# Kernel optimization log

Measured on AMD Instinct MI355X. Metric: run time of the kernel, lower is better.

## Reference

```python
import math
import jax, jax.numpy as jnp
import numpy as np

STEP, BSIZE, NNOD, DIM, HID = 32, 4096, 8, 64, 64


def setup_inputs() -> dict:
    key = jax.random.key(0)
    ks = jax.random.split(key, 9)
    s = 1.0 / math.sqrt(HID)  # torch default uniform init scale
    inp = {
        "input": jax.random.normal(ks[0], (STEP, BSIZE, NNOD, DIM), dtype=jnp.float32),
        "time_dis": jax.random.uniform(ks[1], (BSIZE, STEP), dtype=jnp.float32) * 5.0,
        "w_ih": jax.random.uniform(ks[2], (4 * HID, DIM), jnp.float32, -s, s),
        "w_hh": jax.random.uniform(ks[3], (4 * HID, HID), jnp.float32, -s, s),
        "b_ih": jax.random.uniform(ks[4], (4 * HID,), jnp.float32, -s, s),
        "b_hh": jax.random.uniform(ks[5], (4 * HID,), jnp.float32, -s, s),
        "fc2_w": jax.random.uniform(ks[6], (1, HID), jnp.float32, -s, s),
        "fc2_b": jax.random.uniform(ks[7], (1,), jnp.float32, -s, s),
        "baseline": jnp.array([-30.0], dtype=jnp.float32),
    }
    return inp


def reference(input, time_dis, w_ih, w_hh, b_ih, b_hh, fc2_w, fc2_b, baseline):
    step, bsize, num_nodule, dim = input.shape
    bn = bsize * num_nodule
    x = input.reshape(step, bn, dim)                       # [S, B*N, D]
    # time_dis: [B, S] -> expand over nodules -> [S, B*N]
    td = jnp.broadcast_to(time_dis[:, :, None], (bsize, step, num_nodule))
    td = jnp.transpose(td, (1, 0, 2)).reshape(step, bn)
    # original loop: step 0 uses td[0], step i>0 uses td[i-1]
    td_used = jnp.concatenate([td[:1], td[:-1]], axis=0)   # [S, B*N]

    hid = w_hh.shape[1]
    h0 = jnp.zeros((bn, hid), dtype=input.dtype)
    c0 = jnp.zeros((bn, hid), dtype=input.dtype)

    def cell(carry, step_in):
        h, c = carry
        x_t, t_t = step_in
        gates = x_t @ w_ih.T + b_ih + h @ w_hh.T + b_hh    # [B*N, 4H]
        i_g, f_g, g_g, o_g = jnp.split(gates, 4, axis=-1)
        i_g = jax.nn.sigmoid(i_g)
        f_g = jax.nn.sigmoid(f_g)
        g_g = jnp.tanh(g_g)
        o_g = jax.nn.sigmoid(o_g)
        # time-distanced decay on the retained cell memory: 1/log(e + dt)
        decay = (1.0 / jnp.log(math.e + t_t))[:, None]
        c_new = f_g * decay * c + i_g * g_g
        h_new = o_g * jnp.tanh(c_new)
        return (h_new, c_new), None

    (hx, cx), _ = jax.lax.scan(cell, (h0, c0), (x, td_used))

    out2 = jax.nn.sigmoid(hx @ fc2_w.T + fc2_b).reshape(bsize, num_nodule)
    base_prob = jax.nn.sigmoid(baseline)[0]
    # noisy-OR pooling over nodules plus learned baseline leak
    casePred = 1.0 - jnp.prod(1.0 - out2, axis=1) * (1.0 - base_prob)
    return casePred
```

## Files before the change

kernel.cpp:

```cpp
#include <hip/hip_runtime.h>
#include <hip/hip_bf16.h>
#include <math.h>


#define STEPS 32
#define BSIZE 4096
#define NNOD  8
#define DIMK  64
#define HIDK  64
#define BN    (BSIZE * NNOD)
#define ROWS  64
#define NBLK  (BN / ROWS)

typedef __attribute__((ext_vector_type(8))) short short8;
typedef __attribute__((ext_vector_type(4))) float f32x4;

__device__ __forceinline__ unsigned short f2bf(float f) {
    union { float f; unsigned u; } v; v.f = f;
    unsigned r = v.u + 0x7fffu + ((v.u >> 16) & 1u);
    return (unsigned short)(r >> 16);
}
__device__ __forceinline__ float bf2f(unsigned short h) {
    union { unsigned u; float f; } v; v.u = ((unsigned)h) << 16;
    return v.f;
}
__device__ __forceinline__ float fast_sigmoid(float x) {
    float e = __builtin_amdgcn_exp2f(-1.44269504f * x);
    return __builtin_amdgcn_rcpf(1.0f + e);
}
__device__ __forceinline__ float fast_tanh(float x) {
    float e = __builtin_amdgcn_exp2f(2.88539008f * x);
    return 1.0f - 2.0f * __builtin_amdgcn_rcpf(e + 1.0f);
}

__global__ __launch_bounds__(256, 2)
void disrnn_kernel(const float* __restrict__ x,
                   const float* __restrict__ time_dis,
                   const float* __restrict__ w_ih,
                   const float* __restrict__ w_hh,
                   const float* __restrict__ b_ih,
                   const float* __restrict__ b_hh,
                   const float* __restrict__ fc2_w,
                   const float* __restrict__ fc2_b,
                   const float* __restrict__ baseline,
                   float* __restrict__ out)
{
    __shared__ unsigned short sX[ROWS * 64];
    __shared__ unsigned short sH[ROWS * 64];
    __shared__ float sDecay[8 * STEPS];

    const int tid  = threadIdx.x;
    const int wave = tid >> 6;
    const int lane = tid & 63;
    const int l15  = lane & 15;
    const int lk   = lane >> 4;
    const int blk  = blockIdx.x;
    const int row0 = blk * ROWS;

    {
        int g = tid >> 5, st = tid & 31;
        int b = blk * 8 + g;
        float td = time_dis[b * STEPS + (st == 0 ? 0 : st - 1)];
        sDecay[g * STEPS + st] = __builtin_amdgcn_rcpf(logf(2.71828182845904523f + td));
    }
    for (int i = tid; i < ROWS * 64; i += 256) sH[i] = 0;

    short8 bwih[4][2], bwhh[4][2];
    float  biasv[4];
    #pragma unroll
    for (int q = 0; q < 4; ++q) {
        int n = q * 64 + wave * 16 + l15;
        biasv[q] = b_ih[n] + b_hh[n];
        #pragma unroll
        for (int kk = 0; kk < 2; ++kk) {
            int k0 = kk * 32 + lk * 8;
            short8 vi, vh;
            #pragma unroll
            for (int j = 0; j < 8; ++j) {
                vi[j] = (short)f2bf(w_ih[n * 64 + k0 + j]);
                vh[j] = (short)f2bf(w_hh[n * 64 + k0 + j]);
            }
            bwih[q][kk] = vi;
            bwhh[q][kk] = vh;
        }
    }

    float c[4][4];
    #pragma unroll
    for (int m = 0; m < 4; ++m)
        #pragma unroll
        for (int j = 0; j < 4; ++j) c[m][j] = 0.0f;

    __syncthreads();

    for (int s = 0; s < STEPS; ++s) {
        const float* Xs = x + ((size_t)s * BN + row0) * DIMK;
        #pragma unroll
        for (int it = 0; it < 2; ++it) {
            int gg = it * 256 + tid;
            int r  = gg >> 3, ch = gg & 7;
            const float4* src = (const float4*)(Xs + r * 64 + ch * 8);
            float4 a = src[0], b2 = src[1];
            short8 v;
            v[0] = (short)f2bf(a.x);  v[1] = (short)f2bf(a.y);
            v[2] = (short)f2bf(a.z);  v[3] = (short)f2bf(a.w);
            v[4] = (short)f2bf(b2.x); v[5] = (short)f2bf(b2.y);
            v[6] = (short)f2bf(b2.z); v[7] = (short)f2bf(b2.w);
            *(short8*)&sX[r * 64 + ((ch ^ (r & 7)) * 8)] = v;
        }
        __syncthreads();

        f32x4 acc[4][4];
        #pragma unroll
        for (int m = 0; m < 4; ++m) {
            int rl = m * 16 + l15;
            int sw = rl & 7;
            short8 ax0 = *(const short8*)&sX[rl * 64 + (((0 + lk) ^ sw) * 8)];
            short8 ax1 = *(const short8*)&sX[rl * 64 + (((4 + lk) ^ sw) * 8)];
            short8 ah0 = *(const short8*)&sH[rl * 64 + (((0 + lk) ^ sw) * 8)];
            short8 ah1 = *(const short8*)&sH[rl * 64 + (((4 + lk) ^ sw) * 8)];
            #pragma unroll
            for (int q = 0; q < 4; ++q) {
                f32x4 a0 = {biasv[q], biasv[q], biasv[q], biasv[q]};
                a0 = __builtin_amdgcn_mfma_f32_16x16x32_bf16(ax0, bwih[q][0], a0, 0, 0, 0);
                a0 = __builtin_amdgcn_mfma_f32_16x16x32_bf16(ax1, bwih[q][1], a0, 0, 0, 0);
                a0 = __builtin_amdgcn_mfma_f32_16x16x32_bf16(ah0, bwhh[q][0], a0, 0, 0, 0);
                a0 = __builtin_amdgcn_mfma_f32_16x16x32_bf16(ah1, bwhh[q][1], a0, 0, 0, 0);
                acc[m][q] = a0;
            }
        }
        __syncthreads();

        #pragma unroll
        for (int m = 0; m < 4; ++m) {
            #pragma unroll
            for (int j = 0; j < 4; ++j) {
                int rl = m * 16 + lk * 4 + j;
                float decay = sDecay[(rl >> 3) * STEPS + s];
                float ig = fast_sigmoid(acc[m][0][j]);
                float fg = fast_sigmoid(acc[m][1][j]);
                float g2 = fast_tanh(acc[m][2][j]);
                float og = fast_sigmoid(acc[m][3][j]);
                float cn = fg * decay * c[m][j] + ig * g2;
                c[m][j] = cn;
                float hn = og * fast_tanh(cn);
                int col = wave * 16 + l15;
                sH[rl * 64 + (((col >> 3) ^ (rl & 7)) * 8) + (col & 7)] = f2bf(hn);
            }
        }
    }
    __syncthreads();

    if (tid < 64) {
        int r = tid;
        float sum = 0.0f;
        #pragma unroll
        for (int ch = 0; ch < 8; ++ch) {
            short8 v = *(const short8*)&sH[r * 64 + ((ch ^ (r & 7)) * 8)];
            #pragma unroll
            for (int j = 0; j < 8; ++j)
                sum += bf2f((unsigned short)v[j]) * fc2_w[ch * 8 + j];
        }
        float p  = fast_sigmoid(sum + fc2_b[0]);
        float qv = 1.0f - p;
        qv *= __shfl_xor(qv, 1);
        qv *= __shfl_xor(qv, 2);
        qv *= __shfl_xor(qv, 4);
        if ((tid & 7) == 0) {
            float bp = fast_sigmoid(baseline[0]);
            out[blk * 8 + (tid >> 3)] = 1.0f - qv * (1.0f - bp);
        }
    }
}

extern "C" void kernel_launch(void* const* d_in, const int* in_sizes, int n_in,
                              void* d_out, int out_size, void* d_ws, size_t ws_size,
                              hipStream_t stream) {
    const float* x        = (const float*)d_in[0];
    const float* time_dis = (const float*)d_in[1];
    const float* w_ih     = (const float*)d_in[2];
    const float* w_hh     = (const float*)d_in[3];
    const float* b_ih     = (const float*)d_in[4];
    const float* b_hh     = (const float*)d_in[5];
    const float* fc2_w    = (const float*)d_in[6];
    const float* fc2_b    = (const float*)d_in[7];
    const float* baseline = (const float*)d_in[8];
    float* out = (float*)d_out;

    disrnn_kernel<<<dim3(NBLK), dim3(256), 0, stream>>>(
        x, time_dis, w_ih, w_hh, b_ih, b_hh, fc2_w, fc2_b, baseline, out);
}
```

Baseline: 398.6 us.

## Prefetch next timestep input into registers and use LDS-only barriers

Loads the next step's x tile into registers while the current step computes, then converts and stores it to LDS at the top of the following iteration. Replaces __syncthreads with a barrier that waits only on LDS counters, so the in-flight global prefetch is not drained at each sync. Also hoists the decay lookup out of the inner loop. Adds register pressure under the 2-blocks-per-CU launch bound.

```diff
diff --git a/kernel.cpp b/kernel.cpp
--- a/kernel.cpp
+++ b/kernel.cpp
@@ -31,6 +31,11 @@
 __device__ __forceinline__ float fast_tanh(float x) {
     float e = __builtin_amdgcn_exp2f(2.88539008f * x);
     return 1.0f - 2.0f * __builtin_amdgcn_rcpf(e + 1.0f);
+}
+__device__ __forceinline__ void block_sync_lds() {
+    asm volatile("s_waitcnt lgkmcnt(0)" ::: "memory");
+    __builtin_amdgcn_s_barrier();
+    asm volatile("" ::: "memory");
 }
 
 __global__ __launch_bounds__(256, 2)
@@ -57,6 +62,18 @@
     const int blk  = blockIdx.x;
     const int row0 = blk * ROWS;
 
+    const int r0 = tid >> 3,        c0 = tid & 7;
+    const int r1 = (256 + tid) >> 3, c1 = tid & 7;
+
+    float4 pa0, pa1, pb0, pb1;
+    {
+        const float* Xs = x + (size_t)row0 * DIMK;
+        const float* s0 = Xs + r0 * 64 + c0 * 8;
+        const float* s1 = Xs + r1 * 64 + c1 * 8;
+        pa0 = ((const float4*)s0)[0]; pa1 = ((const float4*)s0)[1];
+        pb0 = ((const float4*)s1)[0]; pb1 = ((const float4*)s1)[1];
+    }
+
     {
         int g = tid >> 5, st = tid & 31;
         int b = blk * 8 + g;
@@ -91,24 +108,31 @@
         #pragma unroll
         for (int j = 0; j < 4; ++j) c[m][j] = 0.0f;
 
-    __syncthreads();
+    block_sync_lds();
 
     for (int s = 0; s < STEPS; ++s) {
-        const float* Xs = x + ((size_t)s * BN + row0) * DIMK;
-        #pragma unroll
-        for (int it = 0; it < 2; ++it) {
-            int gg = it * 256 + tid;
-            int r  = gg >> 3, ch = gg & 7;
-            const float4* src = (const float4*)(Xs + r * 64 + ch * 8);
-            float4 a = src[0], b2 = src[1];
+        {
             short8 v;
-            v[0] = (short)f2bf(a.x);  v[1] = (short)f2bf(a.y);
-            v[2] = (short)f2bf(a.z);  v[3] = (short)f2bf(a.w);
-            v[4] = (short)f2bf(b2.x); v[5] = (short)f2bf(b2.y);
-            v[6] = (short)f2bf(b2.z); v[7] = (short)f2bf(b2.w);
-            *(short8*)&sX[r * 64 + ((ch ^ (r & 7)) * 8)] = v;
-        }
-        __syncthreads();
+            v[0] = (short)f2bf(pa0.x); v[1] = (short)f2bf(pa0.y);
+            v[2] = (short)f2bf(pa0.z); v[3] = (short)f2bf(pa0.w);
+            v[4] = (short)f2bf(pa1.x); v[5] = (short)f2bf(pa1.y);
+            v[6] = (short)f2bf(pa1.z); v[7] = (short)f2bf(pa1.w);
+            *(short8*)&sX[r0 * 64 + ((c0 ^ (r0 & 7)) * 8)] = v;
+            short8 w2;
+            w2[0] = (short)f2bf(pb0.x); w2[1] = (short)f2bf(pb0.y);
+            w2[2] = (short)f2bf(pb0.z); w2[3] = (short)f2bf(pb0.w);
+            w2[4] = (short)f2bf(pb1.x); w2[5] = (short)f2bf(pb1.y);
+            w2[6] = (short)f2bf(pb1.z); w2[7] = (short)f2bf(pb1.w);
+            *(short8*)&sX[r1 * 64 + ((c1 ^ (r1 & 7)) * 8)] = w2;
+        }
+        if (s + 1 < STEPS) {
+            const float* Xs = x + ((size_t)(s + 1) * BN + row0) * DIMK;
+            const float* s0 = Xs + r0 * 64 + c0 * 8;
+            const float* s1 = Xs + r1 * 64 + c1 * 8;
+            pa0 = ((const float4*)s0)[0]; pa1 = ((const float4*)s0)[1];
+            pb0 = ((const float4*)s1)[0]; pb1 = ((const float4*)s1)[1];
+        }
+        block_sync_lds();
 
         f32x4 acc[4][4];
         #pragma unroll
@@ -129,14 +153,14 @@
                 acc[m][q] = a0;
             }
         }
-        __syncthreads();
+        block_sync_lds();
 
         #pragma unroll
         for (int m = 0; m < 4; ++m) {
+            const float decay = sDecay[(m * 2 + (lk >> 1)) * STEPS + s];
             #pragma unroll
             for (int j = 0; j < 4; ++j) {
                 int rl = m * 16 + lk * 4 + j;
-                float decay = sDecay[(rl >> 3) * STEPS + s];
                 float ig = fast_sigmoid(acc[m][0][j]);
                 float fg = fast_sigmoid(acc[m][1][j]);
                 float g2 = fast_tanh(acc[m][2][j]);
@@ -149,7 +173,7 @@
             }
         }
     }
-    __syncthreads();
+    block_sync_lds();
 
     if (tid < 64) {
         int r = tid;
```

Measured after the change: 383.2 us. 3.9% less time.
